# Kernel tuning notes

Hardware: AMD Instinct MI355X
Metric: run time of the kernel (lower is better)

Reference implementation:

```python
import jax, jax.numpy as jnp
import numpy as np

WIN = 11      # window_size
SIGMA = 1.5
CH = 1        # channel
LEVELS = 5
C1 = 0.01 ** 2
C2 = 0.03 ** 2
MS_WEIGHTS = np.array([0.0448, 0.2856, 0.3001, 0.2363, 0.1333], dtype=np.float32)


def _gaussian_window(dtype):
    x = jnp.arange(WIN, dtype=jnp.float32) - WIN // 2
    g = jnp.exp(-(x ** 2) / (2.0 * SIGMA ** 2))
    g = g / g.sum()
    w2 = jnp.outer(g, g)  # [K, K]
    # depthwise kernel [C, 1, K, K]
    return jnp.broadcast_to(w2[None, None], (CH, 1, WIN, WIN)).astype(dtype)


def _blur(x, w):
    # depthwise 11x11 Gaussian blur, SAME padding (= pad window_size//2)
    return jax.lax.conv_general_dilated(
        x, w, window_strides=(1, 1), padding='SAME',
        dimension_numbers=('NCHW', 'OIHW', 'NCHW'),
        feature_group_count=CH)


def _ssim_level(img1, img2, w):
    mu1 = _blur(img1, w)
    mu2 = _blur(img2, w)
    mu1_sq = mu1 * mu1
    mu2_sq = mu2 * mu2
    mu1_mu2 = mu1 * mu2
    sigma1_sq = _blur(img1 * img1, w) - mu1_sq
    sigma2_sq = _blur(img2 * img2, w) - mu2_sq
    sigma12 = _blur(img1 * img2, w) - mu1_mu2
    denom_c = sigma1_sq + sigma2_sq + C2
    mcs_map = (2.0 * sigma12 + C2) / denom_c
    ssim_map = ((2.0 * mu1_mu2 + C1) / (mu1_sq + mu2_sq + C1)) * mcs_map
    return ssim_map.mean(), mcs_map.mean()


def _avg_pool2(x):
    B, C, H, W = x.shape
    return x.reshape(B, C, H // 2, 2, W // 2, 2).mean(axis=(3, 5))


def reference(img1, img2):
    w = _gaussian_window(img1.dtype)
    weights = jnp.asarray(MS_WEIGHTS, dtype=img1.dtype)
    mssim, mcs = [], []
    for _ in range(LEVELS):  # small fixed loop over pyramid levels
        s, m = _ssim_level(img1, img2, w)
        mssim.append(s)
        mcs.append(m)
        img1 = _avg_pool2(img1)
        img2 = _avg_pool2(img2)
    mssim = jnp.stack(mssim)
    mcs = jnp.stack(mcs)
    return jnp.prod(mcs[:LEVELS - 1] ** weights[:LEVELS - 1]) * mssim[LEVELS - 1] ** weights[LEVELS - 1]


def setup_inputs() -> dict:
    key = jax.random.key(0)
    k1, k2 = jax.random.split(key)
    img1 = jax.random.uniform(k1, (32, 1, 512, 512), dtype=jnp.float32)
    # correlated second image so ssim/mcs means stay positive (fractional powers)
    img2 = jnp.clip(img1 + 0.1 * jax.random.normal(k2, img1.shape, dtype=jnp.float32), 0.0, 1.0)
    return {"img1": img1, "img2": img2}
```

## Files before the change

### kernel.cpp

```cpp
#include <hip/hip_runtime.h>
#include <math.h>


typedef float v2f __attribute__((ext_vector_type(2)));

#define TILE 32
#define HALO 5
#define SROWS 42
#define NSLOT 64

struct GaussW { float w[11]; };

#define C1_ (0.01f * 0.01f)
#define C2_ (0.03f * 0.03f)

#define SMEM_FLOATS 6728

__device__ __forceinline__ void ssim_tile(
        const float* __restrict__ p1, const float* __restrict__ p2,
        int W, int tile_x, int tile_y, const GaussW& gw,
        float* __restrict__ accL, unsigned slot, float* smem, int tid) {
    v2f* hb01 = (v2f*)smem;
    v2f* hb23 = (v2f*)(smem + 2 * SROWS * TILE);
    float* hb4 = smem + 4 * SROWS * TILE;
    float* red = smem + 5 * SROWS * TILE;

    const bool xfast = (tile_x >= 8) && (tile_x + TILE + 8 <= W);

    for (int it = tid; it < SROWS * 8; it += 256) {
        int r = it >> 3, c4 = it & 7;
        int gy = tile_y + r - HALO;
        int gx0 = tile_x + (c4 << 2) - 8;
        bool rowok = (gy >= 0) && (gy < W);
        const float* row1 = p1 + (size_t)gy * W;
        const float* row2 = p2 + (size_t)gy * W;
        float a1[20], a2[20];
#pragma unroll
        for (int i = 0; i < 20; i++) { a1[i] = 0.f; a2[i] = 0.f; }
        if (xfast) {
            if (rowok) {
#pragma unroll
                for (int q = 0; q < 5; q++) {
                    float4 v1 = *(const float4*)(row1 + gx0 + q * 4);
                    float4 v2v = *(const float4*)(row2 + gx0 + q * 4);
                    a1[q*4+0] = v1.x;  a1[q*4+1] = v1.y;  a1[q*4+2] = v1.z;  a1[q*4+3] = v1.w;
                    a2[q*4+0] = v2v.x; a2[q*4+1] = v2v.y; a2[q*4+2] = v2v.z; a2[q*4+3] = v2v.w;
                }
            }
        } else {
#pragma unroll
            for (int q = 0; q < 5; q++) {
                int g = gx0 + q * 4;
                if (rowok && g >= 0 && g + 4 <= W) {
                    float4 v1 = *(const float4*)(row1 + g);
                    float4 v2v = *(const float4*)(row2 + g);
                    a1[q*4+0] = v1.x;  a1[q*4+1] = v1.y;  a1[q*4+2] = v1.z;  a1[q*4+3] = v1.w;
                    a2[q*4+0] = v2v.x; a2[q*4+1] = v2v.y; a2[q*4+2] = v2v.z; a2[q*4+3] = v2v.w;
                }
            }
        }
        v2f A[20];
#pragma unroll
        for (int i = 0; i < 20; i++) A[i] = (v2f){a1[i], a2[i]};
        v2f P[14];
        float p12[14];
#pragma unroll
        for (int i = 0; i < 14; i++) {
            v2f u = A[i + 3];
            P[i] = u * u;
            p12[i] = u.x * u.y;
        }
        v2f h01[4] = {(v2f)(0.f), (v2f)(0.f), (v2f)(0.f), (v2f)(0.f)};
        v2f h23[4] = {(v2f)(0.f), (v2f)(0.f), (v2f)(0.f), (v2f)(0.f)};
        float h4[4] = {0.f, 0.f, 0.f, 0.f};
#pragma unroll
        for (int k = 0; k < 11; k++) {
            float wk = gw.w[k];
#pragma unroll
            for (int j = 0; j < 4; j++) {
                h01[j] += wk * A[3 + j + k];
                h23[j] += wk * P[j + k];
                h4[j]  += wk * p12[j + k];
            }
        }
        int ob = r * TILE + (c4 << 2);
#pragma unroll
        for (int j = 0; j < 4; j++) { hb01[ob + j] = h01[j]; hb23[ob + j] = h23[j]; }
        *(float4*)&hb4[ob] = make_float4(h4[0], h4[1], h4[2], h4[3]);
    }
    __syncthreads();

    float ssim_v = 0.f, mcs_v = 0.f;
    {
        int tx = tid & 31, y0 = (tid >> 5) * 4;
        v2f m01[4], m23[4];
        float m4[4];
        {
            v2f v[14];
#pragma unroll
            for (int r = 0; r < 14; r++) v[r] = hb01[(y0 + r) * TILE + tx];
#pragma unroll
            for (int j = 0; j < 4; j++) {
                v2f s = (v2f)(0.f);
#pragma unroll
                for (int k = 0; k < 11; k++) s += gw.w[k] * v[j + k];
                m01[j] = s;
            }
        }
        {
            v2f v[14];
#pragma unroll
            for (int r = 0; r < 14; r++) v[r] = hb23[(y0 + r) * TILE + tx];
#pragma unroll
            for (int j = 0; j < 4; j++) {
                v2f s = (v2f)(0.f);
#pragma unroll
                for (int k = 0; k < 11; k++) s += gw.w[k] * v[j + k];
                m23[j] = s;
            }
        }
        {
            float v[14];
#pragma unroll
            for (int r = 0; r < 14; r++) v[r] = hb4[(y0 + r) * TILE + tx];
#pragma unroll
            for (int j = 0; j < 4; j++) {
                float s = 0.f;
#pragma unroll
                for (int k = 0; k < 11; k++) s += gw.w[k] * v[j + k];
                m4[j] = s;
            }
        }
#pragma unroll
        for (int j = 0; j < 4; j++) {
            float mu1 = m01[j].x, mu2 = m01[j].y;
            float mu1sq = mu1 * mu1, mu2sq = mu2 * mu2, mu12 = mu1 * mu2;
            float sg11 = m23[j].x - mu1sq;
            float sg22 = m23[j].y - mu2sq;
            float sg12 = m4[j] - mu12;
            float mcs  = (2.f * sg12 + C2_) / (sg11 + sg22 + C2_);
            float ssim = ((2.f * mu12 + C1_) / (mu1sq + mu2sq + C1_)) * mcs;
            ssim_v += ssim;
            mcs_v  += mcs;
        }
    }

#pragma unroll
    for (int off = 32; off > 0; off >>= 1) {
        ssim_v += __shfl_down(ssim_v, off);
        mcs_v  += __shfl_down(mcs_v, off);
    }
    int wave = tid >> 6, lane = tid & 63;
    if (lane == 0) { red[wave] = ssim_v; red[4 + wave] = mcs_v; }
    __syncthreads();
    if (tid == 0) {
        float S = red[0] + red[1] + red[2] + red[3];
        float M = red[4] + red[5] + red[6] + red[7];
        atomicAdd(&accL[slot], S);
        atomicAdd(&accL[NSLOT + slot], M);
    }
}

__device__ __forceinline__ void pyramid_region(
        const float* __restrict__ in1, const float* __restrict__ in2,
        int n, int reg,
        float* __restrict__ l1a, float* __restrict__ l1b,
        float* __restrict__ l2a, float* __restrict__ l2b,
        float* __restrict__ l3a, float* __restrict__ l3b,
        float* __restrict__ l4a, float* __restrict__ l4b,
        float* smem, int tid) {
    float* b1 = smem;
    float* b2 = smem + 1024;
    float* c1 = smem + 2048;
    float* c2 = smem + 2304;
    float* d1 = smem + 2560;
    float* d2 = smem + 2624;
    const int rx = reg & 7, ry = reg >> 3;
    const float* p1 = in1 + (size_t)n * 512 * 512;
    const float* p2 = in2 + (size_t)n * 512 * 512;

    for (int i = tid; i < 32 * 16; i += 256) {
        int oy = i >> 4, oxp = i & 15;
        int gy = ry * 64 + 2 * oy, gx = rx * 64 + 4 * oxp;
        float4 r10 = *(const float4*)(p1 + (size_t)gy * 512 + gx);
        float4 r11 = *(const float4*)(p1 + (size_t)(gy + 1) * 512 + gx);
        float4 r20 = *(const float4*)(p2 + (size_t)gy * 512 + gx);
        float4 r21 = *(const float4*)(p2 + (size_t)(gy + 1) * 512 + gx);
        float2 o1 = make_float2(0.25f * (r10.x + r10.y + r11.x + r11.y),
                                0.25f * (r10.z + r10.w + r11.z + r11.w));
        float2 o2 = make_float2(0.25f * (r20.x + r20.y + r21.x + r21.y),
                                0.25f * (r20.z + r20.w + r21.z + r21.w));
        *(float2*)&b1[oy * 32 + 2 * oxp] = o1;
        *(float2*)&b2[oy * 32 + 2 * oxp] = o2;
        size_t o = (size_t)n * 256 * 256 + (size_t)(ry * 32 + oy) * 256 + rx * 32 + 2 * oxp;
        *(float2*)&l1a[o] = o1;
        *(float2*)&l1b[o] = o2;
    }
    __syncthreads();
    if (tid < 16 * 8) {
        int oy = tid >> 3, oxp = tid & 7;
        float4 r10 = *(const float4*)&b1[(2 * oy) * 32 + 4 * oxp];
        float4 r11 = *(const float4*)&b1[(2 * oy + 1) * 32 + 4 * oxp];
        float4 r20 = *(const float4*)&b2[(2 * oy) * 32 + 4 * oxp];
        float4 r21 = *(const float4*)&b2[(2 * oy + 1) * 32 + 4 * oxp];
        float2 o1 = make_float2(0.25f * (r10.x + r10.y + r11.x + r11.y),
                                0.25f * (r10.z + r10.w + r11.z + r11.w));
        float2 o2 = make_float2(0.25f * (r20.x + r20.y + r21.x + r21.y),
                                0.25f * (r20.z + r20.w + r21.z + r21.w));
        *(float2*)&c1[oy * 16 + 2 * oxp] = o1;
        *(float2*)&c2[oy * 16 + 2 * oxp] = o2;
        size_t o = (size_t)n * 128 * 128 + (size_t)(ry * 16 + oy) * 128 + rx * 16 + 2 * oxp;
        *(float2*)&l2a[o] = o1;
        *(float2*)&l2b[o] = o2;
    }
    __syncthreads();
    if (tid < 8 * 4) {
        int oy = tid >> 2, oxp = tid & 3;
        float4 r10 = *(const float4*)&c1[(2 * oy) * 16 + 4 * oxp];
        float4 r11 = *(const float4*)&c1[(2 * oy + 1) * 16 + 4 * oxp];
        float4 r20 = *(const float4*)&c2[(2 * oy) * 16 + 4 * oxp];
        float4 r21 = *(const float4*)&c2[(2 * oy + 1) * 16 + 4 * oxp];
        float2 o1 = make_float2(0.25f * (r10.x + r10.y + r11.x + r11.y),
                                0.25f * (r10.z + r10.w + r11.z + r11.w));
        float2 o2 = make_float2(0.25f * (r20.x + r20.y + r21.x + r21.y),
                                0.25f * (r20.z + r20.w + r21.z + r21.w));
        *(float2*)&d1[oy * 8 + 2 * oxp] = o1;
        *(float2*)&d2[oy * 8 + 2 * oxp] = o2;
        size_t o = (size_t)n * 64 * 64 + (size_t)(ry * 8 + oy) * 64 + rx * 8 + 2 * oxp;
        *(float2*)&l3a[o] = o1;
        *(float2*)&l3b[o] = o2;
    }
    __syncthreads();
    if (tid < 4 * 2) {
        int oy = tid >> 1, oxp = tid & 1;
        float4 r10 = *(const float4*)&d1[(2 * oy) * 8 + 4 * oxp];
        float4 r11 = *(const float4*)&d1[(2 * oy + 1) * 8 + 4 * oxp];
        float4 r20 = *(const float4*)&d2[(2 * oy) * 8 + 4 * oxp];
        float4 r21 = *(const float4*)&d2[(2 * oy + 1) * 8 + 4 * oxp];
        float2 o1 = make_float2(0.25f * (r10.x + r10.y + r11.x + r11.y),
                                0.25f * (r10.z + r10.w + r11.z + r11.w));
        float2 o2 = make_float2(0.25f * (r20.x + r20.y + r21.x + r21.y),
                                0.25f * (r20.z + r20.w + r21.z + r21.w));
        size_t o = (size_t)n * 32 * 32 + (size_t)(ry * 4 + oy) * 32 + rx * 4 + 2 * oxp;
        *(float2*)&l4a[o] = o1;
        *(float2*)&l4b[o] = o2;
    }
}

__global__ __launch_bounds__(256, 4) void d1_kernel(
        const float* __restrict__ i0a, const float* __restrict__ i0b,
        float* __restrict__ l1a, float* __restrict__ l1b,
        float* __restrict__ l2a, float* __restrict__ l2b,
        float* __restrict__ l3a, float* __restrict__ l3b,
        float* __restrict__ l4a, float* __restrict__ l4b,
        float* __restrict__ acc, GaussW gw) {
    __shared__ float smem[SMEM_FLOATS];
    const int tid = threadIdx.x;
    const int t = blockIdx.x;
    const int n = blockIdx.y;
    if (t < 64) {
        pyramid_region(i0a, i0b, n, t, l1a, l1b, l2a, l2b, l3a, l3b, l4a, l4b,
                       smem, tid);
    } else {
        int idx = t - 64;
        int tile_x = (idx & 15) << 5;
        int tile_y = (idx >> 4) << 5;
        const float* p1 = i0a + (size_t)n * 512 * 512;
        const float* p2 = i0b + (size_t)n * 512 * 512;
        unsigned slot = ((unsigned)(idx << 5) + (unsigned)n) & (NSLOT - 1);
        ssim_tile(p1, p2, 512, tile_x, tile_y, gw, acc, slot, smem, tid);
    }
}

__global__ __launch_bounds__(256, 4) void d2_kernel(
        const float* __restrict__ l1a, const float* __restrict__ l1b,
        const float* __restrict__ l2a, const float* __restrict__ l2b,
        const float* __restrict__ l3a, const float* __restrict__ l3b,
        const float* __restrict__ l4a, const float* __restrict__ l4b,
        float* __restrict__ acc, GaussW gw) {
    __shared__ float smem[SMEM_FLOATS];
    const int tid = threadIdx.x;
    const int t = blockIdx.x;
    const int n = blockIdx.y;
    int level, idx, W;
    const float* base1;
    const float* base2;
    if (t < 64)      { level = 1; idx = t;      W = 256; base1 = l1a; base2 = l1b; }
    else if (t < 80) { level = 2; idx = t - 64; W = 128; base1 = l2a; base2 = l2b; }
    else if (t < 84) { level = 3; idx = t - 80; W = 64;  base1 = l3a; base2 = l3b; }
    else             { level = 4; idx = 0;      W = 32;  base1 = l4a; base2 = l4b; }
    const int tpr = W >> 5;
    const int sh = 31 - __clz(tpr);
    const int tile_x = (idx & (tpr - 1)) << 5;
    const int tile_y = (idx >> sh) << 5;
    const float* p1 = base1 + (size_t)n * W * W;
    const float* p2 = base2 + (size_t)n * W * W;
    unsigned slot = ((unsigned)(t << 5) + (unsigned)n) & (NSLOT - 1);
    ssim_tile(p1, p2, W, tile_x, tile_y, gw, acc + level * 2 * NSLOT, slot,
              smem, tid);
}

__global__ void finalize_kernel(const float* __restrict__ acc,
                                float* __restrict__ out, int N) {
    int lane = threadIdx.x & 63;
    float sums[10];
#pragma unroll
    for (int q = 0; q < 10; q++) {
        float v = acc[q * NSLOT + lane];
#pragma unroll
        for (int off = 32; off > 0; off >>= 1) v += __shfl_down(v, off);
        sums[q] = v;
    }
    if (blockIdx.x == 0 && threadIdx.x == 0) {
        const float wts[5] = {0.0448f, 0.2856f, 0.3001f, 0.2363f, 0.1333f};
        float r = 1.f;
#pragma unroll
        for (int l = 0; l < 5; l++) {
            int Hl = 512 >> l;
            float cnt = (float)N * (float)Hl * (float)Hl;
            float ssim_m = sums[2 * l] / cnt;
            float mcs_m  = sums[2 * l + 1] / cnt;
            if (l < 4) r *= powf(mcs_m, wts[l]);
            else       r *= powf(ssim_m, wts[4]);
        }
        out[0] = r;
    }
}

extern "C" void kernel_launch(void* const* d_in, const int* in_sizes, int n_in,
                              void* d_out, int out_size, void* d_ws, size_t ws_size,
                              hipStream_t stream) {
    const float* img1 = (const float*)d_in[0];
    const float* img2 = (const float*)d_in[1];
    float* out = (float*)d_out;
    const int HW0 = 512 * 512;
    const int N = in_sizes[0] / HW0;

    float* base = (float*)d_ws;
    float* acc = base;
    size_t cur = 10 * NSLOT;
    float* w1[5] = {nullptr};
    float* w2[5] = {nullptr};
    for (int l = 1; l < 5; l++) {
        int Hl = 512 >> l;
        size_t hw = (size_t)Hl * Hl;
        w1[l] = base + cur; cur += (size_t)N * hw;
        w2[l] = base + cur; cur += (size_t)N * hw;
    }

    hipMemsetAsync(acc, 0, 10 * NSLOT * sizeof(float), stream);

    GaussW gw;
    {
        double g[11], sum = 0.0;
        for (int i = 0; i < 11; i++) {
            double x = (double)(i - 5);
            g[i] = exp(-(x * x) / (2.0 * 1.5 * 1.5));
            sum += g[i];
        }
        for (int i = 0; i < 11; i++) gw.w[i] = (float)(g[i] / sum);
    }

    d1_kernel<<<dim3(320, N), 256, 0, stream>>>(
        img1, img2, w1[1], w2[1], w1[2], w2[2], w1[3], w2[3], w1[4], w2[4],
        acc, gw);
    d2_kernel<<<dim3(85, N), 256, 0, stream>>>(
        w1[1], w2[1], w1[2], w2[2], w1[3], w2[3], w1[4], w2[4], acc, gw);
    finalize_kernel<<<1, 64, 0, stream>>>(acc, out, N);
}
```

Measured before the change: 173.1 us.

## Compute level-1 SSIM in first kernel by pooling on the fly; drop atomics

```diff
diff --git a/kernel.cpp b/kernel.cpp
--- a/kernel.cpp
+++ b/kernel.cpp
@@ -7,19 +7,18 @@
 #define TILE 32
 #define HALO 5
 #define SROWS 42
-#define NSLOT 64
+#define SMEM_FLOATS 6728
 
 struct GaussW { float w[11]; };
 
 #define C1_ (0.01f * 0.01f)
 #define C2_ (0.03f * 0.03f)
 
-#define SMEM_FLOATS 6728
-
 __device__ __forceinline__ void ssim_tile(
         const float* __restrict__ p1, const float* __restrict__ p2,
-        int W, int tile_x, int tile_y, const GaussW& gw,
-        float* __restrict__ accL, unsigned slot, float* smem, int tid) {
+        int W, int W0, bool poolL0,
+        int tile_x, int tile_y, const GaussW& gw,
+        float2* __restrict__ resslot, float* smem, int tid) {
     v2f* hb01 = (v2f*)smem;
     v2f* hb23 = (v2f*)(smem + 2 * SROWS * TILE);
     float* hb4 = smem + 4 * SROWS * TILE;
@@ -32,30 +31,60 @@
         int gy = tile_y + r - HALO;
         int gx0 = tile_x + (c4 << 2) - 8;
         bool rowok = (gy >= 0) && (gy < W);
-        const float* row1 = p1 + (size_t)gy * W;
-        const float* row2 = p2 + (size_t)gy * W;
         float a1[20], a2[20];
 #pragma unroll
         for (int i = 0; i < 20; i++) { a1[i] = 0.f; a2[i] = 0.f; }
-        if (xfast) {
-            if (rowok) {
+        if (!poolL0) {
+            const float* row1 = p1 + (size_t)gy * W;
+            const float* row2 = p2 + (size_t)gy * W;
+            if (xfast) {
+                if (rowok) {
+#pragma unroll
+                    for (int q = 0; q < 5; q++) {
+                        float4 v1 = *(const float4*)(row1 + gx0 + q * 4);
+                        float4 v2v = *(const float4*)(row2 + gx0 + q * 4);
+                        a1[q*4+0] = v1.x;  a1[q*4+1] = v1.y;  a1[q*4+2] = v1.z;  a1[q*4+3] = v1.w;
+                        a2[q*4+0] = v2v.x; a2[q*4+1] = v2v.y; a2[q*4+2] = v2v.z; a2[q*4+3] = v2v.w;
+                    }
+                }
+            } else {
 #pragma unroll
                 for (int q = 0; q < 5; q++) {
-                    float4 v1 = *(const float4*)(row1 + gx0 + q * 4);
-                    float4 v2v = *(const float4*)(row2 + gx0 + q * 4);
-                    a1[q*4+0] = v1.x;  a1[q*4+1] = v1.y;  a1[q*4+2] = v1.z;  a1[q*4+3] = v1.w;
-                    a2[q*4+0] = v2v.x; a2[q*4+1] = v2v.y; a2[q*4+2] = v2v.z; a2[q*4+3] = v2v.w;
+                    int g = gx0 + q * 4;
+                    if (rowok && g >= 0 && g + 4 <= W) {
+                        float4 v1 = *(const float4*)(row1 + g);
+                        float4 v2v = *(const float4*)(row2 + g);
+                        a1[q*4+0] = v1.x;  a1[q*4+1] = v1.y;  a1[q*4+2] = v1.z;  a1[q*4+3] = v1.w;
+                        a2[q*4+0] = v2v.x; a2[q*4+1] = v2v.y; a2[q*4+2] = v2v.z; a2[q*4+3] = v2v.w;
+                    }
                 }
             }
         } else {
+            const float* r10 = p1 + (size_t)(2 * gy) * W0;
+            const float* r11 = r10 + W0;
+            const float* r20 = p2 + (size_t)(2 * gy) * W0;
+            const float* r21 = r20 + W0;
 #pragma unroll
             for (int q = 0; q < 5; q++) {
                 int g = gx0 + q * 4;
-                if (rowok && g >= 0 && g + 4 <= W) {
-                    float4 v1 = *(const float4*)(row1 + g);
-                    float4 v2v = *(const float4*)(row2 + g);
-                    a1[q*4+0] = v1.x;  a1[q*4+1] = v1.y;  a1[q*4+2] = v1.z;  a1[q*4+3] = v1.w;
-                    a2[q*4+0] = v2v.x; a2[q*4+1] = v2v.y; a2[q*4+2] = v2v.z; a2[q*4+3] = v2v.w;
+                bool ok = rowok && (xfast || (g >= 0 && g + 4 <= W));
+                if (ok) {
+                    float4 f0 = *(const float4*)(r10 + 2 * g);
+                    float4 f1 = *(const float4*)(r10 + 2 * g + 4);
+                    float4 f2 = *(const float4*)(r11 + 2 * g);
+                    float4 f3 = *(const float4*)(r11 + 2 * g + 4);
+                    a1[q*4+0] = 0.25f * (f0.x + f0.y + f2.x + f2.y);
+                    a1[q*4+1] = 0.25f * (f0.z + f0.w + f2.z + f2.w);
+                    a1[q*4+2] = 0.25f * (f1.x + f1.y + f3.x + f3.y);
+                    a1[q*4+3] = 0.25f * (f1.z + f1.w + f3.z + f3.w);
+                    float4 g0 = *(const float4*)(r20 + 2 * g);
+                    float4 g1 = *(const float4*)(r20 + 2 * g + 4);
+                    float4 g2 = *(const float4*)(r21 + 2 * g);
+                    float4 g3 = *(const float4*)(r21 + 2 * g + 4);
+                    a2[q*4+0] = 0.25f * (g0.x + g0.y + g2.x + g2.y);
+                    a2[q*4+1] = 0.25f * (g0.z + g0.w + g2.z + g2.w);
+                    a2[q*4+2] = 0.25f * (g1.x + g1.y + g3.x + g3.y);
+                    a2[q*4+3] = 0.25f * (g1.z + g1.w + g3.z + g3.w);
                 }
             }
         }
@@ -156,15 +185,13 @@
     if (tid == 0) {
         float S = red[0] + red[1] + red[2] + red[3];
         float M = red[4] + red[5] + red[6] + red[7];
-        atomicAdd(&accL[slot], S);
-        atomicAdd(&accL[NSLOT + slot], M);
+        *resslot = make_float2(S, M);
     }
 }
 
 __device__ __forceinline__ void pyramid_region(
         const float* __restrict__ in1, const float* __restrict__ in2,
         int n, int reg,
-        float* __restrict__ l1a, float* __restrict__ l1b,
         float* __restrict__ l2a, float* __restrict__ l2b,
         float* __restrict__ l3a, float* __restrict__ l3b,
         float* __restrict__ l4a, float* __restrict__ l4b,
@@ -186,15 +213,12 @@
         float4 r11 = *(const float4*)(p1 + (size_t)(gy + 1) * 512 + gx);
         float4 r20 = *(const float4*)(p2 + (size_t)gy * 512 + gx);
         float4 r21 = *(const float4*)(p2 + (size_t)(gy + 1) * 512 + gx);
-        float2 o1 = make_float2(0.25f * (r10.x + r10.y + r11.x + r11.y),
-                                0.25f * (r10.z + r10.w + r11.z + r11.w));
-        float2 o2 = make_float2(0.25f * (r20.x + r20.y + r21.x + r21.y),
-                                0.25f * (r20.z + r20.w + r21.z + r21.w));
-        *(float2*)&b1[oy * 32 + 2 * oxp] = o1;
-        *(float2*)&b2[oy * 32 + 2 * oxp] = o2;
-        size_t o = (size_t)n * 256 * 256 + (size_t)(ry * 32 + oy) * 256 + rx * 32 + 2 * oxp;
-        *(float2*)&l1a[o] = o1;
-        *(float2*)&l1b[o] = o2;
+        *(float2*)&b1[oy * 32 + 2 * oxp] =
+            make_float2(0.25f * (r10.x + r10.y + r11.x + r11.y),
+                        0.25f * (r10.z + r10.w + r11.z + r11.w));
+        *(float2*)&b2[oy * 32 + 2 * oxp] =
+            make_float2(0.25f * (r20.x + r20.y + r21.x + r21.y),
+                        0.25f * (r20.z + r20.w + r21.z + r21.w));
     }
     __syncthreads();
     if (tid < 16 * 8) {
@@ -249,77 +273,87 @@
 
 __global__ __launch_bounds__(256, 4) void d1_kernel(
         const float* __restrict__ i0a, const float* __restrict__ i0b,
-        float* __restrict__ l1a, float* __restrict__ l1b,
         float* __restrict__ l2a, float* __restrict__ l2b,
         float* __restrict__ l3a, float* __restrict__ l3b,
         float* __restrict__ l4a, float* __restrict__ l4b,
-        float* __restrict__ acc, GaussW gw) {
+        float2* __restrict__ res0, float2* __restrict__ res1, GaussW gw) {
     __shared__ float smem[SMEM_FLOATS];
     const int tid = threadIdx.x;
     const int t = blockIdx.x;
     const int n = blockIdx.y;
+    const float* p1 = i0a + (size_t)n * 512 * 512;
+    const float* p2 = i0b + (size_t)n * 512 * 512;
     if (t < 64) {
-        pyramid_region(i0a, i0b, n, t, l1a, l1b, l2a, l2b, l3a, l3b, l4a, l4b,
-                       smem, tid);
+        pyramid_region(i0a, i0b, n, t, l2a, l2b, l3a, l3b, l4a, l4b, smem, tid);
+    } else if (t < 320) {
+        int idx = t - 64;
+        ssim_tile(p1, p2, 512, 512, false, (idx & 15) << 5, (idx >> 4) << 5,
+                  gw, &res0[n * 256 + idx], smem, tid);
     } else {
-        int idx = t - 64;
-        int tile_x = (idx & 15) << 5;
-        int tile_y = (idx >> 4) << 5;
-        const float* p1 = i0a + (size_t)n * 512 * 512;
-        const float* p2 = i0b + (size_t)n * 512 * 512;
-        unsigned slot = ((unsigned)(idx << 5) + (unsigned)n) & (NSLOT - 1);
-        ssim_tile(p1, p2, 512, tile_x, tile_y, gw, acc, slot, smem, tid);
+        int idx = t - 320;
+        ssim_tile(p1, p2, 256, 512, true, (idx & 7) << 5, (idx >> 3) << 5,
+                  gw, &res1[n * 64 + idx], smem, tid);
     }
 }
 
 __global__ __launch_bounds__(256, 4) void d2_kernel(
-        const float* __restrict__ l1a, const float* __restrict__ l1b,
         const float* __restrict__ l2a, const float* __restrict__ l2b,
         const float* __restrict__ l3a, const float* __restrict__ l3b,
         const float* __restrict__ l4a, const float* __restrict__ l4b,
-        float* __restrict__ acc, GaussW gw) {
+        float2* __restrict__ res2, float2* __restrict__ res3,
+        float2* __restrict__ res4, GaussW gw) {
     __shared__ float smem[SMEM_FLOATS];
     const int tid = threadIdx.x;
     const int t = blockIdx.x;
     const int n = blockIdx.y;
-    int level, idx, W;
-    const float* base1;
-    const float* base2;
-    if (t < 64)      { level = 1; idx = t;      W = 256; base1 = l1a; base2 = l1b; }
-    else if (t < 80) { level = 2; idx = t - 64; W = 128; base1 = l2a; base2 = l2b; }
-    else if (t < 84) { level = 3; idx = t - 80; W = 64;  base1 = l3a; base2 = l3b; }
-    else             { level = 4; idx = 0;      W = 32;  base1 = l4a; base2 = l4b; }
-    const int tpr = W >> 5;
-    const int sh = 31 - __clz(tpr);
-    const int tile_x = (idx & (tpr - 1)) << 5;
-    const int tile_y = (idx >> sh) << 5;
-    const float* p1 = base1 + (size_t)n * W * W;
-    const float* p2 = base2 + (size_t)n * W * W;
-    unsigned slot = ((unsigned)(t << 5) + (unsigned)n) & (NSLOT - 1);
-    ssim_tile(p1, p2, W, tile_x, tile_y, gw, acc + level * 2 * NSLOT, slot,
-              smem, tid);
-}
-
-__global__ void finalize_kernel(const float* __restrict__ acc,
+    const float* b1;
+    const float* b2;
+    int W, tx, ty;
+    float2* slot;
+    if (t < 16)      { W = 128; b1 = l2a; b2 = l2b; tx = (t & 3) << 5; ty = (t >> 2) << 5; slot = &res2[n * 16 + t]; }
+    else if (t < 20) { int i = t - 16; W = 64; b1 = l3a; b2 = l3b; tx = (i & 1) << 5; ty = (i >> 1) << 5; slot = &res3[n * 4 + i]; }
+    else             { W = 32; b1 = l4a; b2 = l4b; tx = 0; ty = 0; slot = &res4[n]; }
+    ssim_tile(b1 + (size_t)n * W * W, b2 + (size_t)n * W * W, W, W, false,
+              tx, ty, gw, slot, smem, tid);
+}
+
+__global__ void finalize_kernel(const float2* __restrict__ res0,
+                                const float2* __restrict__ res1,
+                                const float2* __restrict__ res2,
+                                const float2* __restrict__ res3,
+                                const float2* __restrict__ res4,
                                 float* __restrict__ out, int N) {
-    int lane = threadIdx.x & 63;
-    float sums[10];
-#pragma unroll
-    for (int q = 0; q < 10; q++) {
-        float v = acc[q * NSLOT + lane];
-#pragma unroll
-        for (int off = 32; off > 0; off >>= 1) v += __shfl_down(v, off);
-        sums[q] = v;
-    }
-    if (blockIdx.x == 0 && threadIdx.x == 0) {
+    __shared__ float2 redf[5][4];
+    const int tid = threadIdx.x;
+    const float2* rr[5] = {res0, res1, res2, res3, res4};
+    const int cnts[5] = {N * 256, N * 64, N * 16, N * 4, N};
+#pragma unroll
+    for (int l = 0; l < 5; l++) {
+        float sx = 0.f, sy = 0.f;
+        for (int i = tid; i < cnts[l]; i += 256) {
+            float2 v = rr[l][i];
+            sx += v.x;
+            sy += v.y;
+        }
+#pragma unroll
+        for (int off = 32; off > 0; off >>= 1) {
+            sx += __shfl_down(sx, off);
+            sy += __shfl_down(sy, off);
+        }
+        if ((tid & 63) == 0) redf[l][tid >> 6] = make_float2(sx, sy);
+    }
+    __syncthreads();
+    if (tid == 0) {
         const float wts[5] = {0.0448f, 0.2856f, 0.3001f, 0.2363f, 0.1333f};
         float r = 1.f;
 #pragma unroll
         for (int l = 0; l < 5; l++) {
+            float sx = redf[l][0].x + redf[l][1].x + redf[l][2].x + redf[l][3].x;
+            float sy = redf[l][0].y + redf[l][1].y + redf[l][2].y + redf[l][3].y;
             int Hl = 512 >> l;
             float cnt = (float)N * (float)Hl * (float)Hl;
-            float ssim_m = sums[2 * l] / cnt;
-            float mcs_m  = sums[2 * l + 1] / cnt;
+            float ssim_m = sx / cnt;
+            float mcs_m  = sy / cnt;
             if (l < 4) r *= powf(mcs_m, wts[l]);
             else       r *= powf(ssim_m, wts[4]);
         }
@@ -337,18 +371,18 @@
     const int N = in_sizes[0] / HW0;
 
     float* base = (float*)d_ws;
-    float* acc = base;
-    size_t cur = 10 * NSLOT;
-    float* w1[5] = {nullptr};
-    float* w2[5] = {nullptr};
-    for (int l = 1; l < 5; l++) {
-        int Hl = 512 >> l;
-        size_t hw = (size_t)Hl * Hl;
-        w1[l] = base + cur; cur += (size_t)N * hw;
-        w2[l] = base + cur; cur += (size_t)N * hw;
-    }
-
-    hipMemsetAsync(acc, 0, 10 * NSLOT * sizeof(float), stream);
+    size_t cur = 0;
+    float* l2a = base + cur; cur += (size_t)N * 128 * 128;
+    float* l2b = base + cur; cur += (size_t)N * 128 * 128;
+    float* l3a = base + cur; cur += (size_t)N * 64 * 64;
+    float* l3b = base + cur; cur += (size_t)N * 64 * 64;
+    float* l4a = base + cur; cur += (size_t)N * 32 * 32;
+    float* l4b = base + cur; cur += (size_t)N * 32 * 32;
+    float2* res0 = (float2*)(base + cur); cur += (size_t)N * 512;
+    float2* res1 = (float2*)(base + cur); cur += (size_t)N * 128;
+    float2* res2 = (float2*)(base + cur); cur += (size_t)N * 32;
+    float2* res3 = (float2*)(base + cur); cur += (size_t)N * 8;
+    float2* res4 = (float2*)(base + cur); cur += (size_t)N * 2;
 
     GaussW gw;
     {
@@ -361,10 +395,9 @@
         for (int i = 0; i < 11; i++) gw.w[i] = (float)(g[i] / sum);
     }
 
-    d1_kernel<<<dim3(320, N), 256, 0, stream>>>(
-        img1, img2, w1[1], w2[1], w1[2], w2[2], w1[3], w2[3], w1[4], w2[4],
-        acc, gw);
-    d2_kernel<<<dim3(85, N), 256, 0, stream>>>(
-        w1[1], w2[1], w1[2], w2[2], w1[3], w2[3], w1[4], w2[4], acc, gw);
-    finalize_kernel<<<1, 64, 0, stream>>>(acc, out, N);
-}
+    d1_kernel<<<dim3(384, N), 256, 0, stream>>>(
+        img1, img2, l2a, l2b, l3a, l3b, l4a, l4b, res0, res1, gw);
+    d2_kernel<<<dim3(21, N), 256, 0, stream>>>(
+        l2a, l2b, l3a, l3b, l4a, l4b, res2, res3, res4, gw);
+    finalize_kernel<<<1, 256, 0, stream>>>(res0, res1, res2, res3, res4, out, N);
+}
```

New measurement: 186.0 us. 7.5% more time.
